# Optimization experiments

Hardware: AMD Instinct MI355X
Metric: run time of the kernel (lower is better)

Reference implementation:

```python
import jax, jax.numpy as jnp
import numpy as np

B, N, D, H = 4, 2048, 1024, 8
HD = D // H  # head_dim = 128
TEMPER = 1.0
LN_EPS = 1e-5


def setup_inputs() -> dict:
    key = jax.random.key(0)
    ks = jax.random.split(key, 6)
    return {
        "h": jax.random.normal(ks[0], (B, N, D), dtype=jnp.float32),
        "Wl": jax.random.normal(ks[1], (D, D), dtype=jnp.float32) * (D ** -0.5),
        "Wr": jax.random.normal(ks[2], (D, D), dtype=jnp.float32) * (D ** -0.5),
        "att_l": jax.random.normal(ks[3], (1, HD), dtype=jnp.float32) * (HD ** -0.5),
        "att_r": jax.random.normal(ks[4], (1, HD), dtype=jnp.float32) * (HD ** -0.5),
        "Wf": jax.random.normal(ks[5], (D, D), dtype=jnp.float32) * (D ** -0.5),
        "ln_gamma": jnp.ones((D,), dtype=jnp.float32),
        "ln_beta": jnp.zeros((D,), dtype=jnp.float32),
    }


def _leaky(x):
    return jnp.where(x > 0, x, 0.01 * x)


def reference(h, Wl, Wr, att_l, att_r, Wf, ln_gamma, ln_beta):
    b, n, d = h.shape
    # projections -> [B, H, N, HD]
    fl = (h @ Wl.T).reshape(b, n, H, HD).transpose(0, 2, 1, 3)
    fr = (h @ Wr.T).reshape(b, n, H, HD).transpose(0, 2, 1, 3)
    # additive (GAT-style) scores: sl[b,h,i] + sr[b,h,j]
    sl = jnp.einsum("bhnd,d->bhn", _leaky(fl), att_l[0])
    sr = jnp.einsum("bhnd,d->bhn", _leaky(fr), att_r[0])
    score = (sl[:, :, :, None] + sr[:, :, None, :]) / TEMPER  # [B,H,N,N]
    p = jax.nn.softmax(score, axis=-1)
    # context and merge heads
    ctx = jnp.einsum("bhnm,bhmd->bhnd", p, fr)
    h_sa = ctx.transpose(0, 2, 1, 3).reshape(b, n, d)
    fh = h_sa @ Wf.T
    y = h + fh
    mu = jnp.mean(y, axis=-1, keepdims=True)
    var = jnp.mean(jnp.square(y - mu), axis=-1, keepdims=True)
    return (y - mu) * jax.lax.rsqrt(var + LN_EPS) * ln_gamma + ln_beta
```

## Files before the change

kernel.cpp:

```cpp
#include <hip/hip_runtime.h>
#include <hip/hip_bf16.h>

#define B_ 4
#define N_ 2048
#define D_ 1024
#define H_ 8
#define HD_ 128

typedef __attribute__((ext_vector_type(4))) float f32x4;
typedef __attribute__((ext_vector_type(8))) short bf16x8;

__device__ __forceinline__ short f2bf(float f) {
    unsigned u = __builtin_bit_cast(unsigned, f);
    u = (u + 0x7FFFu + ((u >> 16) & 1u)) >> 16;
    return (short)u;
}
__device__ __forceinline__ float bf2f(unsigned short s) {
    unsigned u = (unsigned)s << 16;
    return __builtin_bit_cast(float, u);
}

typedef const __attribute__((address_space(1))) void* gas_t;
typedef __attribute__((address_space(3))) void* las_t;

__device__ __forceinline__ void gload16(const void* g, void* l) {
    __builtin_amdgcn_global_load_lds((gas_t)g, (las_t)l, 16, 0, 0);
}

__global__ __launch_bounds__(256) void k_cvt(
    const float* __restrict__ h, short* __restrict__ hb,
    const float* __restrict__ Wr, short* __restrict__ wrb)
{
    int blk = blockIdx.x;
    const float* src;
    short* dst;
    int i;
    if (blk < 4096) { src = h;  dst = hb;  i = blk * 256 + threadIdx.x; }
    else            { src = Wr; dst = wrb; i = (blk - 4096) * 256 + threadIdx.x; }
    float4 a = ((const float4*)src)[i * 2];
    float4 b = ((const float4*)src)[i * 2 + 1];
    bf16x8 o;
    o[0] = f2bf(a.x); o[1] = f2bf(a.y); o[2] = f2bf(a.z); o[3] = f2bf(a.w);
    o[4] = f2bf(b.x); o[5] = f2bf(b.y); o[6] = f2bf(b.z); o[7] = f2bf(b.w);
    ((bf16x8*)dst)[i] = o;
}

__global__ __launch_bounds__(256) void k_proj_sr(
    const short* __restrict__ hb, const short* __restrict__ wrb,
    const float* __restrict__ att_r, float* __restrict__ sr)
{
    __shared__ short sA[64 * 32];
    __shared__ short sB[128 * 32];
    __shared__ float part[4][64];

    const int tid  = threadIdx.x;
    const int lane = tid & 63;
    const int wave = tid >> 6;
    const int cc   = lane & 15;
    const int g    = lane >> 4;
    const int rowBase = blockIdx.x * 64;
    const int head    = blockIdx.y;

    const int srow = lane >> 2;
    const int scol = (lane & 3) * 8;
    const short* gA0 = hb  + (size_t)(rowBase + wave * 16 + srow) * D_ + scol;
    const short* gB0 = wrb + (size_t)(head * HD_ + wave * 32 + srow) * D_ + scol;
    const short* gB1 = gB0 + (size_t)16 * D_;
    char* lA = (char*)sA + wave * 1024;
    char* lB = (char*)sB + wave * 2048;

    f32x4 acc[4][2];
#pragma unroll
    for (int m = 0; m < 4; ++m)
#pragma unroll
        for (int n = 0; n < 2; ++n) acc[m][n] = (f32x4){0.f, 0.f, 0.f, 0.f};

    for (int k0 = 0; k0 < D_; k0 += 32) {
        gload16(gA0 + k0, lA);
        gload16(gB0 + k0, lB);
        gload16(gB1 + k0, lB + 1024);
        __syncthreads();

        bf16x8 aF[4], bF[2];
#pragma unroll
        for (int m = 0; m < 4; ++m)
            aF[m] = *(const bf16x8*)(sA + (m * 16 + cc) * 32 + g * 8);
#pragma unroll
        for (int n = 0; n < 2; ++n)
            bF[n] = *(const bf16x8*)(sB + (wave * 32 + n * 16 + cc) * 32 + g * 8);
#pragma unroll
        for (int m = 0; m < 4; ++m)
#pragma unroll
            for (int n = 0; n < 2; ++n)
                acc[m][n] = __builtin_amdgcn_mfma_f32_16x16x32_bf16(
                    aF[m], bF[n], acc[m][n], 0, 0, 0);
        __syncthreads();
    }

    float ar[2];
#pragma unroll
    for (int n = 0; n < 2; ++n) ar[n] = att_r[wave * 32 + n * 16 + cc];

#pragma unroll
    for (int m = 0; m < 4; ++m) {
#pragma unroll
        for (int r = 0; r < 4; ++r) {
            float p = 0.f;
#pragma unroll
            for (int n = 0; n < 2; ++n) {
                float v = acc[m][n][r];
                v = v > 0.f ? v : 0.01f * v;
                p += v * ar[n];
            }
            p += __shfl_xor(p, 1); p += __shfl_xor(p, 2);
            p += __shfl_xor(p, 4); p += __shfl_xor(p, 8);
            if (cc == 0) part[wave][m * 16 + g * 4 + r] = p;
        }
    }
    __syncthreads();
    if (tid < 64) {
        const int grow = rowBase + tid;
        const int b = grow >> 11, j = grow & (N_ - 1);
        sr[(size_t)(b * H_ + head) * N_ + j] =
            part[0][tid] + part[1][tid] + part[2][tid] + part[3][tid];
    }
}

__global__ __launch_bounds__(256) void k_hbar(
    const short* __restrict__ hbm, const float* __restrict__ sr,
    float* __restrict__ hp)
{
    const int dc = blockIdx.x;
    const int jc = blockIdx.y;
    const int b  = blockIdx.z;
    const int tid = threadIdx.x;
    const int d = dc * 256 + tid;

    __shared__ float smx[8], sism[8];
    {
        const int hh = tid >> 5;
        const int sl = tid & 31;
        const float4* row = (const float4*)(sr + (size_t)(b * H_ + hh) * N_);
        float4 v[16];
        float mx = -1e30f;
#pragma unroll
        for (int k = 0; k < 16; ++k) {
            v[k] = row[sl + k * 32];
            mx = fmaxf(fmaxf(mx, fmaxf(v[k].x, v[k].y)), fmaxf(v[k].z, v[k].w));
        }
#pragma unroll
        for (int m = 1; m < 32; m <<= 1) mx = fmaxf(mx, __shfl_xor(mx, m));
        float sum = 0.f;
#pragma unroll
        for (int k = 0; k < 16; ++k)
            sum += expf(v[k].x - mx) + expf(v[k].y - mx) +
                   expf(v[k].z - mx) + expf(v[k].w - mx);
#pragma unroll
        for (int m = 1; m < 32; m <<= 1) sum += __shfl_xor(sum, m);
        if (sl == 0) { smx[hh] = mx; sism[hh] = 1.f / sum; }
    }
    __syncthreads();

    __shared__ float wl[8][128];
    for (int idx = tid; idx < 1024; idx += 256) {
        const int hh = idx >> 7, jj = idx & 127;
        wl[hh][jj] = expf(sr[(size_t)(b * H_ + hh) * N_ + jc * 128 + jj]
                          - smx[hh]) * sism[hh];
    }
    __syncthreads();

    float acc[8] = {0.f, 0.f, 0.f, 0.f, 0.f, 0.f, 0.f, 0.f};
    const short* hp0 = hbm + ((size_t)(b * N_ + jc * 128)) * D_ + d;
    for (int jj = 0; jj < 128; ++jj) {
        float hv = bf2f((unsigned short)hp0[(size_t)jj * D_]);
#pragma unroll
        for (int hh = 0; hh < 8; ++hh) acc[hh] += wl[hh][jj] * hv;
    }
#pragma unroll
    for (int hh = 0; hh < 8; ++hh)
        hp[((size_t)(jc * 32) + b * 8 + hh) * D_ + d] = acc[hh];
}

__global__ __launch_bounds__(256) void k_ctx(
    const float* __restrict__ hp, const float* __restrict__ Wr,
    float* __restrict__ ctx)
{
    const int bh = blockIdx.x >> 5;
    const int b = bh >> 3, head = bh & 7;
    const int dg = (blockIdx.x & 31) * 4;
    const int tid = threadIdx.x;
    const int lane = tid & 63, wave = tid >> 6;

    __shared__ float xs[1024];
    float4 s = {0.f, 0.f, 0.f, 0.f};
#pragma unroll
    for (int jc = 0; jc < 16; ++jc) {
        float4 v = ((const float4*)(hp + ((size_t)(jc * 32) + bh) * D_))[tid];
        s.x += v.x; s.y += v.y; s.z += v.z; s.w += v.w;
    }
    ((float4*)xs)[tid] = s;
    __syncthreads();

    const int o = dg + wave;
    const float* wrow = Wr + (size_t)(head * HD_ + o) * D_;
    float acc = 0.f;
#pragma unroll
    for (int it = 0; it < 4; ++it) {
        float4 wv = *(const float4*)(wrow + it * 256 + lane * 4);
        float4 xv = ((const float4*)xs)[it * 64 + lane];
        acc += wv.x * xv.x + wv.y * xv.y + wv.z * xv.z + wv.w * xv.w;
    }
#pragma unroll
    for (int m = 1; m < 64; m <<= 1) acc += __shfl_xor(acc, m);
    if (lane == 0) ctx[(size_t)b * D_ + head * HD_ + o] = acc;
}

__global__ __launch_bounds__(256) void k_fvec(
    const float* __restrict__ ctx, const float* __restrict__ Wf,
    float* __restrict__ fvec)
{
    const int o = blockIdx.x * 4 + (threadIdx.x >> 6);
    const int lane = threadIdx.x & 63;
    const int b = o >> 10, orow = o & 1023;
    const float* x  = ctx + (size_t)b * D_;
    const float* wf = Wf + (size_t)orow * D_;
    float s = 0.f;
#pragma unroll
    for (int it = 0; it < 4; ++it) {
        float4 xv = *(const float4*)(x + it * 256 + lane * 4);
        float4 wv = *(const float4*)(wf + it * 256 + lane * 4);
        s += xv.x * wv.x + xv.y * wv.y + xv.z * wv.z + xv.w * wv.w;
    }
#pragma unroll
    for (int m = 1; m < 64; m <<= 1) s += __shfl_xor(s, m);
    if (lane == 0) fvec[o] = s;
}

__global__ __launch_bounds__(256) void k_ln(
    const short* __restrict__ hbm, const float* __restrict__ fvec,
    const float* __restrict__ gamma, const float* __restrict__ beta,
    float* __restrict__ out)
{
    const int row = blockIdx.x;
    const int b = row >> 11;
    const int tid = threadIdx.x;
    const int lane = tid & 63, wave = tid >> 6;

    short4 hv4 = *(const short4*)(hbm + (size_t)row * D_ + tid * 4);
    float4 fv = *(const float4*)(fvec + (size_t)b * D_ + tid * 4);
    const float y0 = bf2f((unsigned short)hv4.x) + fv.x;
    const float y1 = bf2f((unsigned short)hv4.y) + fv.y;
    const float y2 = bf2f((unsigned short)hv4.z) + fv.z;
    const float y3 = bf2f((unsigned short)hv4.w) + fv.w;

    float s = y0 + y1 + y2 + y3;
    float q = y0 * y0 + y1 * y1 + y2 * y2 + y3 * y3;
#pragma unroll
    for (int m = 1; m < 64; m <<= 1) { s += __shfl_xor(s, m); q += __shfl_xor(q, m); }

    __shared__ float rs[4], rq[4];
    if (lane == 0) { rs[wave] = s; rq[wave] = q; }
    __syncthreads();
    s = rs[0] + rs[1] + rs[2] + rs[3];
    q = rq[0] + rq[1] + rq[2] + rq[3];

    const float mu  = s * (1.f / D_);
    const float var = q * (1.f / D_) - mu * mu;
    const float inv = rsqrtf(var + 1e-5f);

    float4 gv = *(const float4*)(gamma + tid * 4);
    float4 bv = *(const float4*)(beta + tid * 4);
    float4 ov;
    ov.x = (y0 - mu) * inv * gv.x + bv.x;
    ov.y = (y1 - mu) * inv * gv.y + bv.y;
    ov.z = (y2 - mu) * inv * gv.z + bv.z;
    ov.w = (y3 - mu) * inv * gv.w + bv.w;
    *(float4*)(out + (size_t)row * D_ + tid * 4) = ov;
}

extern "C" void kernel_launch(void* const* d_in, const int* in_sizes, int n_in,
                              void* d_out, int out_size, void* d_ws, size_t ws_size,
                              hipStream_t stream) {
    const float* h     = (const float*)d_in[0];
    const float* Wr    = (const float*)d_in[2];
    const float* att_r = (const float*)d_in[4];
    const float* Wf    = (const float*)d_in[5];
    const float* gamma = (const float*)d_in[6];
    const float* beta  = (const float*)d_in[7];
    float* out = (float*)d_out;

    char* ws = (char*)d_ws;
    float* sr    = (float*)(ws);
    float* hp    = (float*)(ws + 524288);
    float* ctx   = (float*)(ws + 2752512);
    float* fvec  = (float*)(ws + 2768896);
    short* hb    = (short*)(ws + 4194304);
    short* wrb   = (short*)(ws + 4194304 + 16777216);

    k_cvt<<<4096 + 512, 256, 0, stream>>>(h, hb, Wr, wrb);
    k_proj_sr<<<dim3(B_ * N_ / 64, H_), 256, 0, stream>>>(hb, wrb, att_r, sr);
    k_hbar<<<dim3(4, 16, 4), 256, 0, stream>>>(hb, sr, hp);
    k_ctx<<<1024, 256, 0, stream>>>(hp, Wr, ctx);
    k_fvec<<<1024, 256, 0, stream>>>(ctx, Wf, fvec);
    k_ln<<<B_ * N_, 256, 0, stream>>>(hb, fvec, gamma, beta, out);
}
```

Measured before the change: 77.16 us.

## Double-buffer LDS tiles in projection GEMM and raise MFMA wave priority

Result: no change. 78.20 us (+1.3%).

```diff
diff --git a/kernel.cpp b/kernel.cpp
--- a/kernel.cpp
+++ b/kernel.cpp
@@ -49,8 +49,8 @@
     const short* __restrict__ hb, const short* __restrict__ wrb,
     const float* __restrict__ att_r, float* __restrict__ sr)
 {
-    __shared__ short sA[64 * 32];
-    __shared__ short sB[128 * 32];
+    __shared__ short sA[2][64 * 32];
+    __shared__ short sB[2][128 * 32];
     __shared__ float part[4][64];
 
     const int tid  = threadIdx.x;
@@ -66,8 +66,8 @@
     const short* gA0 = hb  + (size_t)(rowBase + wave * 16 + srow) * D_ + scol;
     const short* gB0 = wrb + (size_t)(head * HD_ + wave * 32 + srow) * D_ + scol;
     const short* gB1 = gB0 + (size_t)16 * D_;
-    char* lA = (char*)sA + wave * 1024;
-    char* lB = (char*)sB + wave * 2048;
+    const int offA = wave * 1024;
+    const int offB = wave * 2048;
 
     f32x4 acc[4][2];
 #pragma unroll
@@ -75,25 +75,36 @@
 #pragma unroll
         for (int n = 0; n < 2; ++n) acc[m][n] = (f32x4){0.f, 0.f, 0.f, 0.f};
 
-    for (int k0 = 0; k0 < D_; k0 += 32) {
-        gload16(gA0 + k0, lA);
-        gload16(gB0 + k0, lB);
-        gload16(gB1 + k0, lB + 1024);
-        __syncthreads();
-
+    gload16(gA0, (char*)sA[0] + offA);
+    gload16(gB0, (char*)sB[0] + offB);
+    gload16(gB1, (char*)sB[0] + offB + 1024);
+    __syncthreads();
+
+    for (int t = 0; t < 32; ++t) {
+        const int cur = t & 1;
+        if (t < 31) {
+            const int k0 = (t + 1) * 32;
+            gload16(gA0 + k0, (char*)sA[cur ^ 1] + offA);
+            gload16(gB0 + k0, (char*)sB[cur ^ 1] + offB);
+            gload16(gB1 + k0, (char*)sB[cur ^ 1] + offB + 1024);
+        }
+        const short* bufA = sA[cur];
+        const short* bufB = sB[cur];
         bf16x8 aF[4], bF[2];
 #pragma unroll
         for (int m = 0; m < 4; ++m)
-            aF[m] = *(const bf16x8*)(sA + (m * 16 + cc) * 32 + g * 8);
+            aF[m] = *(const bf16x8*)(bufA + (m * 16 + cc) * 32 + g * 8);
 #pragma unroll
         for (int n = 0; n < 2; ++n)
-            bF[n] = *(const bf16x8*)(sB + (wave * 32 + n * 16 + cc) * 32 + g * 8);
+            bF[n] = *(const bf16x8*)(bufB + (wave * 32 + n * 16 + cc) * 32 + g * 8);
+        __builtin_amdgcn_s_setprio(1);
 #pragma unroll
         for (int m = 0; m < 4; ++m)
 #pragma unroll
             for (int n = 0; n < 2; ++n)
                 acc[m][n] = __builtin_amdgcn_mfma_f32_16x16x32_bf16(
                     aF[m], bF[n], acc[m][n], 0, 0, 0);
+        __builtin_amdgcn_s_setprio(0);
         __syncthreads();
     }
 
@@ -171,6 +182,7 @@
 
     float acc[8] = {0.f, 0.f, 0.f, 0.f, 0.f, 0.f, 0.f, 0.f};
     const short* hp0 = hbm + ((size_t)(b * N_ + jc * 128)) * D_ + d;
+#pragma unroll 4
     for (int jj = 0; jj < 128; ++jj) {
         float hv = bf2f((unsigned short)hp0[(size_t)jj * D_]);
 #pragma unroll
```
